# Performance work log

Hardware: AMD Instinct MI355X
Metric: run time of the kernel (lower is better)

The kernel has to match this reference:

```python
import jax, jax.numpy as jnp
import numpy as np

BN_EPS = 1e-5
RES_SCALE = 0.7


def setup_inputs() -> dict:
    key = jax.random.key(0)
    ks = jax.random.split(key, 10)
    N, IN_DIM, HID, E, L = 50000, 2000, 64, 1600000, 4
    features = jax.random.normal(ks[0], (N, IN_DIM), dtype=jnp.float32)
    edges = jax.random.randint(ks[1], (2, E), 0, N, dtype=jnp.int64)
    # GCNConv params: layer 0 is in_dim->hid, layers 1..3 are hid->hid
    W0 = jax.random.normal(ks[2], (IN_DIM, HID), dtype=jnp.float32) / np.sqrt(IN_DIM)
    b0 = jnp.zeros((HID,), dtype=jnp.float32)
    Wh = jax.random.normal(ks[3], (L - 1, HID, HID), dtype=jnp.float32) / np.sqrt(HID)
    bh = jnp.zeros((L - 1, HID), dtype=jnp.float32)
    # BatchNorm1d affine params per layer
    gamma = jnp.ones((L, HID), dtype=jnp.float32)
    beta = jnp.zeros((L, HID), dtype=jnp.float32)
    # learned layer-mixing weights (torch.randn init)
    lw = jax.random.normal(ks[4], (L,), dtype=jnp.float32)
    return {"features": features, "edges": edges, "W0": W0, "b0": b0,
            "Wh": Wh, "bh": bh, "gamma": gamma, "beta": beta, "lw": lw}


def reference(features, edges, W0, b0, Wh, bh, gamma, beta, lw):
    n = features.shape[0]
    src, dst = edges[0], edges[1]
    # GCN symmetric normalization with self-loops, edge_weight=1
    deg = jnp.zeros((n,), features.dtype).at[dst].add(1.0) + 1.0  # +1 self loop
    dinv = jax.lax.rsqrt(deg)
    enorm = dinv[src] * dinv[dst]       # [E]
    snorm = dinv * dinv                 # [N], self-loop norm

    def gcn_conv(x, W, b):
        xw = x @ W                                            # [N, H]
        agg = jnp.zeros_like(xw).at[dst].add(xw[src] * enorm[:, None])
        agg = agg + xw * snorm[:, None]
        return agg + b

    def batchnorm(x, g, bt):
        m = x.mean(axis=0)
        v = x.var(axis=0)  # biased variance, as in BN training normalization
        return (x - m) * jax.lax.rsqrt(v + BN_EPS) * g + bt

    L = gamma.shape[0]
    Ws = [W0] + [Wh[i] for i in range(L - 1)]
    bs = [b0] + [bh[i] for i in range(L - 1)]

    layer_out = []
    x = features
    for i in range(L):
        x = gcn_conv(x, Ws[i], bs[i])
        x = jax.nn.relu(batchnorm(x, gamma[i], beta[i]))
        if i > 0:
            x = x + RES_SCALE * layer_out[i - 1]
        layer_out.append(x)

    w = jax.nn.softmax(lw)
    emb = layer_out[0] * w[0]
    for i in range(1, L):
        emb = emb + layer_out[i] * w[i]
    return emb
```

## Files before the change

kernel.cpp:

```cpp
#include <hip/hip_runtime.h>
#include <hip/hip_bf16.h>
#include <math.h>

#define BN_EPS 1e-5f
#define RES_SCALE 0.7f

typedef float f4 __attribute__((ext_vector_type(4)));
typedef short s8 __attribute__((ext_vector_type(8)));

__device__ inline short f2bf(float f) {
    __hip_bfloat16 h = __float2bfloat16(f);
    return *reinterpret_cast<short*>(&h);
}

__device__ inline float bf2f(unsigned short u) {
    return __uint_as_float((unsigned)u << 16);
}

__global__ __launch_bounds__(256) void k_zero(int* counts, int* cursor, float* stats, int N, int S) {
    int i = blockIdx.x * 256 + threadIdx.x;
    if (i < N) { counts[i] = 0; cursor[i] = 0; }
    if (i < S) stats[i] = 0.0f;
}

__global__ __launch_bounds__(256) void k_count(const int* __restrict__ edges, int E, int* __restrict__ counts) {
    int e = blockIdx.x * 256 + threadIdx.x;
    if (e < E) atomicAdd(&counts[edges[E + e]], 1);
}

__global__ __launch_bounds__(256) void k_dinv(const int* __restrict__ counts, float* __restrict__ dinv, int N) {
    int i = blockIdx.x * 256 + threadIdx.x;
    if (i < N) dinv[i] = rsqrtf((float)counts[i] + 1.0f);
}

__global__ __launch_bounds__(256) void k_scan1(const int* __restrict__ counts, int* __restrict__ bsum, int N) {
    __shared__ int sd[256];
    int t = threadIdx.x;
    int base = blockIdx.x * 1024 + t * 4;
    int s = 0;
    if (base + 3 < N) { int4 v = *(const int4*)(counts + base); s = v.x + v.y + v.z + v.w; }
    else { for (int j = 0; j < 4; ++j) if (base + j < N) s += counts[base + j]; }
    sd[t] = s; __syncthreads();
    for (int off = 128; off > 0; off >>= 1) { if (t < off) sd[t] += sd[t + off]; __syncthreads(); }
    if (t == 0) bsum[blockIdx.x] = sd[0];
}

__global__ void k_scan2(int* bsum, int B, int* rowstart, int N) {
    if (threadIdx.x == 0 && blockIdx.x == 0) {
        int run = 0;
        for (int b = 0; b < B; ++b) { int v = bsum[b]; bsum[b] = run; run += v; }
        rowstart[N] = run;
    }
}

__global__ __launch_bounds__(256) void k_scan3(const int* __restrict__ counts, const int* __restrict__ bsum,
                                               int* __restrict__ rowstart, int N) {
    __shared__ int sd[256];
    int t = threadIdx.x;
    int base = blockIdx.x * 1024 + t * 4;
    int v0 = 0, v1 = 0, v2 = 0, v3 = 0;
    if (base + 3 < N) { int4 v = *(const int4*)(counts + base); v0 = v.x; v1 = v.y; v2 = v.z; v3 = v.w; }
    else {
        if (base < N) v0 = counts[base];
        if (base + 1 < N) v1 = counts[base + 1];
        if (base + 2 < N) v2 = counts[base + 2];
        if (base + 3 < N) v3 = counts[base + 3];
    }
    int s = v0 + v1 + v2 + v3;
    sd[t] = s; __syncthreads();
    for (int off = 1; off < 256; off <<= 1) {
        int add = (t >= off) ? sd[t - off] : 0;
        __syncthreads();
        sd[t] += add;
        __syncthreads();
    }
    int excl = sd[t] - s + bsum[blockIdx.x];
    if (base < N)     rowstart[base]     = excl;
    if (base + 1 < N) rowstart[base + 1] = excl + v0;
    if (base + 2 < N) rowstart[base + 2] = excl + v0 + v1;
    if (base + 3 < N) rowstart[base + 3] = excl + v0 + v1 + v2;
}

__global__ __launch_bounds__(256) void k_scatter(const int* __restrict__ edges, int E,
                                                 const int* __restrict__ rowstart, int* __restrict__ cursor,
                                                 int* __restrict__ colA) {
    int e = blockIdx.x * 256 + threadIdx.x;
    if (e >= E) return;
    int s = edges[e], d = edges[E + e];
    int pos = rowstart[d] + atomicAdd(&cursor[d], 1);
    colA[pos] = s;
}

__global__ __launch_bounds__(256) void k_wt(const float* __restrict__ W0, const float* __restrict__ Wh,
                                            short* __restrict__ WT0, short* __restrict__ WTh, int K0) {
    __shared__ short Ts[64][72];
    int b = blockIdx.x, t = threadIdx.x;
    int nk0 = (K0 + 63) >> 6;
    const float* W; short* dst; int K, kt;
    if (b < nk0) { W = W0; dst = WT0; K = K0; kt = b * 64; }
    else { int l = b - nk0; W = Wh + (size_t)l * 64 * 64; dst = WTh + (size_t)l * 64 * 64; K = 64; kt = 0; }
    #pragma unroll
    for (int i = 0; i < 16; ++i) {
        int idx = t + i * 256;
        int r = idx >> 6, c = idx & 63;
        int gk = kt + r;
        Ts[c][r] = (gk < K) ? f2bf(W[(size_t)gk * 64 + c]) : (short)0;
    }
    __syncthreads();
    #pragma unroll
    for (int i = 0; i < 16; ++i) {
        int idx = t + i * 256;
        int n = idx >> 6, r = idx & 63;
        int gk = kt + r;
        if (gk < K) dst[(size_t)n * K + gk] = Ts[n][r];
    }
}

__global__ __launch_bounds__(256) void k_mm(const float* __restrict__ X, const short* __restrict__ WT,
                                            const float* __restrict__ dinv,
                                            __hip_bfloat16* __restrict__ Cb, int N, int K) {
    __shared__ float Xs[64][36];
    __shared__ short Ws[64][40];
    int t = threadIdx.x;
    int w = t >> 6, lane = t & 63;
    int m = lane & 15, kq = lane >> 4;
    int row0 = blockIdx.x * 64;

    int xr = t >> 3, xc = t & 7;
    int wn = t >> 2, wc = t & 3;

    f4 acc[4] = {};
    f4 px0, px1; int4 pw;

    {
        int gr0 = row0 + xr, gr1 = row0 + xr + 32, gk = xc * 4;
        px0 = (gr0 < N && gk < K) ? *(const f4*)(X + (size_t)gr0 * K + gk) : (f4){};
        px1 = (gr1 < N && gk < K) ? *(const f4*)(X + (size_t)gr1 * K + gk) : (f4){};
        int gkw = wc * 8;
        pw = (gkw < K) ? *(const int4*)(WT + (size_t)wn * K + gkw) : make_int4(0, 0, 0, 0);
    }

    for (int kt = 0; kt < K; kt += 32) {
        *(f4*)&Xs[xr][xc * 4] = px0;
        *(f4*)&Xs[xr + 32][xc * 4] = px1;
        *(int4*)&Ws[wn][wc * 8] = pw;
        __syncthreads();

        int kn = kt + 32;
        if (kn < K) {
            int gr0 = row0 + xr, gr1 = row0 + xr + 32, gk = kn + xc * 4;
            px0 = (gr0 < N && gk < K) ? *(const f4*)(X + (size_t)gr0 * K + gk) : (f4){};
            px1 = (gr1 < N && gk < K) ? *(const f4*)(X + (size_t)gr1 * K + gk) : (f4){};
            int gkw = kn + wc * 8;
            pw = (gkw < K) ? *(const int4*)(WT + (size_t)wn * K + gkw) : make_int4(0, 0, 0, 0);
        }

        f4 a0 = *(const f4*)&Xs[w * 16 + m][kq * 8];
        f4 a1 = *(const f4*)&Xs[w * 16 + m][kq * 8 + 4];
        s8 av;
        #pragma unroll
        for (int j = 0; j < 4; ++j) { av[j] = f2bf(a0[j]); av[j + 4] = f2bf(a1[j]); }
        #pragma unroll
        for (int ct = 0; ct < 4; ++ct) {
            s8 bv = *(const s8*)&Ws[ct * 16 + m][kq * 8];
            acc[ct] = __builtin_amdgcn_mfma_f32_16x16x32_bf16(av, bv, acc[ct], 0, 0, 0);
        }
        __syncthreads();
    }

    #pragma unroll
    for (int reg = 0; reg < 4; ++reg) {
        int gr = row0 + w * 16 + kq * 4 + reg;
        if (gr < N) {
            float di = dinv[gr];
            #pragma unroll
            for (int ct = 0; ct < 4; ++ct)
                Cb[(size_t)gr * 64 + ct * 16 + m] = __float2bfloat16(acc[ct][reg] * di);
        }
    }
}

__global__ __launch_bounds__(256) void k_gather(const __hip_bfloat16* __restrict__ xw, const int* __restrict__ colA,
                                                const int* __restrict__ rowstart,
                                                const float* __restrict__ dinv, float* __restrict__ agg, int N) {
    int wave = (blockIdx.x * 256 + threadIdx.x) >> 6;
    int lane = threadIdx.x & 63;
    if (wave >= N) return;
    int r = wave;
    const unsigned short* xwu = (const unsigned short*)xw;
    float acc = bf2f(xwu[(size_t)r * 64 + lane]);
    int b = rowstart[r], e = rowstart[r + 1];
    for (int base = b; base < e; base += 64) {
        int idx = base + lane;
        int c = (idx < e) ? colA[idx] : 0;
        int cnt = min(64, e - base);
        int j = 0;
        for (; j + 7 < cnt; j += 8) {
            int s0 = __builtin_amdgcn_readlane(c, j);
            int s1 = __builtin_amdgcn_readlane(c, j + 1);
            int s2 = __builtin_amdgcn_readlane(c, j + 2);
            int s3 = __builtin_amdgcn_readlane(c, j + 3);
            int s4 = __builtin_amdgcn_readlane(c, j + 4);
            int s5 = __builtin_amdgcn_readlane(c, j + 5);
            int s6 = __builtin_amdgcn_readlane(c, j + 6);
            int s7 = __builtin_amdgcn_readlane(c, j + 7);
            float v0 = bf2f(xwu[(size_t)s0 * 64 + lane]);
            float v1 = bf2f(xwu[(size_t)s1 * 64 + lane]);
            float v2 = bf2f(xwu[(size_t)s2 * 64 + lane]);
            float v3 = bf2f(xwu[(size_t)s3 * 64 + lane]);
            float v4 = bf2f(xwu[(size_t)s4 * 64 + lane]);
            float v5 = bf2f(xwu[(size_t)s5 * 64 + lane]);
            float v6 = bf2f(xwu[(size_t)s6 * 64 + lane]);
            float v7 = bf2f(xwu[(size_t)s7 * 64 + lane]);
            acc += ((v0 + v1) + (v2 + v3)) + ((v4 + v5) + (v6 + v7));
        }
        for (; j < cnt; ++j) {
            int s = __builtin_amdgcn_readlane(c, j);
            acc += bf2f(xwu[(size_t)s * 64 + lane]);
        }
    }
    agg[(size_t)r * 64 + lane] = acc * dinv[r];
}

__global__ __launch_bounds__(256) void k_stats(const float* __restrict__ x, float* __restrict__ stats, int N) {
    int col = threadIdx.x & 63;
    int sub = threadIdx.x >> 6;
    float s = 0.f, s2 = 0.f;
    for (int r = blockIdx.x * 4 + sub; r < N; r += gridDim.x * 4) {
        float v = x[(size_t)r * 64 + col];
        s += v; s2 += v * v;
    }
    __shared__ float sd[2][4][64];
    sd[0][sub][col] = s; sd[1][sub][col] = s2;
    __syncthreads();
    if (sub == 0) {
        s  = sd[0][0][col] + sd[0][1][col] + sd[0][2][col] + sd[0][3][col];
        s2 = sd[1][0][col] + sd[1][1][col] + sd[1][2][col] + sd[1][3][col];
        atomicAdd(&stats[col], s);
        atomicAdd(&stats[64 + col], s2);
    }
}

__global__ __launch_bounds__(256) void k_elem(const float* __restrict__ agg, const float* __restrict__ stats,
                                              const float* __restrict__ gamma, const float* __restrict__ beta,
                                              const float* __restrict__ lw, const float* __restrict__ xprev,
                                              float* __restrict__ xcur, float* __restrict__ emb,
                                              int N, int layer, int L) {
    int i = blockIdx.x * 256 + threadIdx.x;
    if (i >= N * 64) return;
    int c = i & 63;
    float rN = 1.0f / (float)N;
    float mn = stats[c] * rN;
    float var = stats[64 + c] * rN - mn * mn;
    float inv = rsqrtf(var + BN_EPS);
    float v = (agg[i] - mn) * inv * gamma[c] + beta[c];
    v = fmaxf(v, 0.0f);
    if (layer > 0) v += RES_SCALE * xprev[i];
    xcur[i] = v;
    float mx = lw[0];
    for (int j = 1; j < L; ++j) mx = fmaxf(mx, lw[j]);
    float sum = 0.f, wl = 0.f;
    for (int j = 0; j < L; ++j) {
        float e = __expf(lw[j] - mx);
        sum += e;
        if (j == layer) wl = e;
    }
    wl /= sum;
    float prev = (layer == 0) ? 0.0f : emb[i];
    emb[i] = prev + wl * v;
}

extern "C" void kernel_launch(void* const* d_in, const int* in_sizes, int n_in,
                              void* d_out, int out_size, void* d_ws, size_t ws_size,
                              hipStream_t stream) {
    const float* features = (const float*)d_in[0];
    const int*   edges    = (const int*)d_in[1];
    const float* W0       = (const float*)d_in[2];
    const float* Wh       = (const float*)d_in[4];
    const float* gamma    = (const float*)d_in[6];
    const float* beta     = (const float*)d_in[7];
    const float* lw       = (const float*)d_in[8];

    const int HID    = in_sizes[3];
    const int IN_DIM = in_sizes[2] / HID;
    const int N      = in_sizes[0] / IN_DIM;
    const int E      = in_sizes[1] / 2;
    const int L      = in_sizes[8];
    float* out = (float*)d_out;

    char* ws = (char*)d_ws;
    auto alloc = [&](size_t bytes) { char* p = ws; ws += (bytes + 255) & ~(size_t)255; return p; };
    int*   counts   = (int*)alloc((size_t)N * 4);
    int*   cursor   = (int*)alloc((size_t)N * 4);
    int*   rowstart = (int*)alloc((size_t)(N + 1) * 4);
    int*   bsum     = (int*)alloc(256 * 4);
    float* dinv     = (float*)alloc((size_t)N * 4);
    float* stats    = (float*)alloc((size_t)L * 128 * 4);
    int*   colA     = (int*)alloc((size_t)E * 4);
    short* WT0      = (short*)alloc((size_t)HID * IN_DIM * 2);
    short* WTh      = (short*)alloc((size_t)(L - 1) * HID * HID * 2);
    __hip_bfloat16* xw = (__hip_bfloat16*)alloc((size_t)N * HID * 2);
    float* agg      = (float*)alloc((size_t)N * HID * 4);
    float* x0       = (float*)alloc((size_t)N * HID * 4);
    float* x1       = (float*)alloc((size_t)N * HID * 4);

    int S = L * 128;
    int zgrid = (max(N, S) + 255) / 256;
    k_zero<<<zgrid, 256, 0, stream>>>(counts, cursor, stats, N, S);

    int egrid = (E + 255) / 256;
    int ngrid = (N + 255) / 256;
    k_count<<<egrid, 256, 0, stream>>>(edges, E, counts);
    k_dinv<<<ngrid, 256, 0, stream>>>(counts, dinv, N);

    int B = (N + 1023) / 1024;
    k_scan1<<<B, 256, 0, stream>>>(counts, bsum, N);
    k_scan2<<<1, 64, 0, stream>>>(bsum, B, rowstart, N);
    k_scan3<<<B, 256, 0, stream>>>(counts, bsum, rowstart, N);
    k_scatter<<<egrid, 256, 0, stream>>>(edges, E, rowstart, cursor, colA);

    int nk0 = (IN_DIM + 63) / 64;
    k_wt<<<nk0 + (L - 1), 256, 0, stream>>>(W0, Wh, WT0, WTh, IN_DIM);

    int mmgrid = (N + 63) / 64;
    int ggrid  = (N + 3) / 4;
    int elgrid = ((size_t)N * HID + 255) / 256;

    const float* xc_prev = nullptr;
    for (int l = 0; l < L; ++l) {
        const float* Xin = (l == 0) ? features : xc_prev;
        int K = (l == 0) ? IN_DIM : HID;
        const short* WTl = (l == 0) ? WT0 : WTh + (size_t)(l - 1) * HID * HID;
        k_mm<<<mmgrid, 256, 0, stream>>>(Xin, WTl, dinv, xw, N, K);
        k_gather<<<ggrid, 256, 0, stream>>>(xw, colA, rowstart, dinv, agg, N);
        k_stats<<<256, 256, 0, stream>>>(agg, stats + l * 128, N);
        float* xcur = (l % 2 == 0) ? x0 : x1;
        const float* xprev = (l == 0) ? nullptr : ((l % 2 == 0) ? x1 : x0);
        k_elem<<<elgrid, 256, 0, stream>>>(agg, stats + l * 128, gamma + l * HID, beta + l * HID,
                                           lw, xprev, xcur, out, N, l, L);
        xc_prev = xcur;
    }
}
```

Baseline: 1.053 ms.

## Pack gather loads in pairs, widen GEMM K-tile, vectorize elementwise, fuse dinv

```diff
diff --git a/kernel.cpp b/kernel.cpp
--- a/kernel.cpp
+++ b/kernel.cpp
@@ -11,10 +11,6 @@
 __device__ inline short f2bf(float f) {
     __hip_bfloat16 h = __float2bfloat16(f);
     return *reinterpret_cast<short*>(&h);
-}
-
-__device__ inline float bf2f(unsigned short u) {
-    return __uint_as_float((unsigned)u << 16);
 }
 
 __global__ __launch_bounds__(256) void k_zero(int* counts, int* cursor, float* stats, int N, int S) {
@@ -28,18 +24,28 @@
     if (e < E) atomicAdd(&counts[edges[E + e]], 1);
 }
 
-__global__ __launch_bounds__(256) void k_dinv(const int* __restrict__ counts, float* __restrict__ dinv, int N) {
-    int i = blockIdx.x * 256 + threadIdx.x;
-    if (i < N) dinv[i] = rsqrtf((float)counts[i] + 1.0f);
-}
-
-__global__ __launch_bounds__(256) void k_scan1(const int* __restrict__ counts, int* __restrict__ bsum, int N) {
+__global__ __launch_bounds__(256) void k_scan1(const int* __restrict__ counts, int* __restrict__ bsum,
+                                               float* __restrict__ dinv, int N) {
     __shared__ int sd[256];
     int t = threadIdx.x;
     int base = blockIdx.x * 1024 + t * 4;
     int s = 0;
-    if (base + 3 < N) { int4 v = *(const int4*)(counts + base); s = v.x + v.y + v.z + v.w; }
-    else { for (int j = 0; j < 4; ++j) if (base + j < N) s += counts[base + j]; }
+    if (base + 3 < N) {
+        int4 v = *(const int4*)(counts + base);
+        s = v.x + v.y + v.z + v.w;
+        f4 d;
+        d.x = rsqrtf((float)v.x + 1.0f);
+        d.y = rsqrtf((float)v.y + 1.0f);
+        d.z = rsqrtf((float)v.z + 1.0f);
+        d.w = rsqrtf((float)v.w + 1.0f);
+        *(f4*)(dinv + base) = d;
+    } else {
+        for (int j = 0; j < 4; ++j) if (base + j < N) {
+            int cv = counts[base + j];
+            s += cv;
+            dinv[base + j] = rsqrtf((float)cv + 1.0f);
+        }
+    }
     sd[t] = s; __syncthreads();
     for (int off = 128; off > 0; off >>= 1) { if (t < off) sd[t] += sd[t + off]; __syncthreads(); }
     if (t == 0) bsum[blockIdx.x] = sd[0];
@@ -119,8 +125,8 @@
 __global__ __launch_bounds__(256) void k_mm(const float* __restrict__ X, const short* __restrict__ WT,
                                             const float* __restrict__ dinv,
                                             __hip_bfloat16* __restrict__ Cb, int N, int K) {
-    __shared__ float Xs[64][36];
-    __shared__ short Ws[64][40];
+    __shared__ float Xs[64][68];
+    __shared__ short Ws[64][72];
     int t = threadIdx.x;
     int w = t >> 6, lane = t & 63;
     int m = lane & 15, kq = lane >> 4;
@@ -130,40 +136,59 @@
     int wn = t >> 2, wc = t & 3;
 
     f4 acc[4] = {};
-    f4 px0, px1; int4 pw;
+    f4 px0, px1, px2, px3; int4 pw0, pw1;
 
     {
-        int gr0 = row0 + xr, gr1 = row0 + xr + 32, gk = xc * 4;
-        px0 = (gr0 < N && gk < K) ? *(const f4*)(X + (size_t)gr0 * K + gk) : (f4){};
-        px1 = (gr1 < N && gk < K) ? *(const f4*)(X + (size_t)gr1 * K + gk) : (f4){};
-        int gkw = wc * 8;
-        pw = (gkw < K) ? *(const int4*)(WT + (size_t)wn * K + gkw) : make_int4(0, 0, 0, 0);
-    }
-
-    for (int kt = 0; kt < K; kt += 32) {
-        *(f4*)&Xs[xr][xc * 4] = px0;
-        *(f4*)&Xs[xr + 32][xc * 4] = px1;
-        *(int4*)&Ws[wn][wc * 8] = pw;
+        int gr0 = row0 + xr, gr1 = row0 + xr + 32;
+        int gk0 = xc * 4, gk1 = 32 + xc * 4;
+        px0 = (gr0 < N && gk0 < K) ? *(const f4*)(X + (size_t)gr0 * K + gk0) : (f4){};
+        px1 = (gr0 < N && gk1 < K) ? *(const f4*)(X + (size_t)gr0 * K + gk1) : (f4){};
+        px2 = (gr1 < N && gk0 < K) ? *(const f4*)(X + (size_t)gr1 * K + gk0) : (f4){};
+        px3 = (gr1 < N && gk1 < K) ? *(const f4*)(X + (size_t)gr1 * K + gk1) : (f4){};
+        int gw0 = wc * 8, gw1 = 32 + wc * 8;
+        pw0 = (gw0 < K) ? *(const int4*)(WT + (size_t)wn * K + gw0) : make_int4(0, 0, 0, 0);
+        pw1 = (gw1 < K) ? *(const int4*)(WT + (size_t)wn * K + gw1) : make_int4(0, 0, 0, 0);
+    }
+
+    for (int kt = 0; kt < K; kt += 64) {
+        *(f4*)&Xs[xr][xc * 4]           = px0;
+        *(f4*)&Xs[xr][32 + xc * 4]      = px1;
+        *(f4*)&Xs[xr + 32][xc * 4]      = px2;
+        *(f4*)&Xs[xr + 32][32 + xc * 4] = px3;
+        *(int4*)&Ws[wn][wc * 8]         = pw0;
+        *(int4*)&Ws[wn][32 + wc * 8]    = pw1;
         __syncthreads();
 
-        int kn = kt + 32;
+        int kn = kt + 64;
         if (kn < K) {
-            int gr0 = row0 + xr, gr1 = row0 + xr + 32, gk = kn + xc * 4;
-            px0 = (gr0 < N && gk < K) ? *(const f4*)(X + (size_t)gr0 * K + gk) : (f4){};
-            px1 = (gr1 < N && gk < K) ? *(const f4*)(X + (size_t)gr1 * K + gk) : (f4){};
-            int gkw = kn + wc * 8;
-            pw = (gkw < K) ? *(const int4*)(WT + (size_t)wn * K + gkw) : make_int4(0, 0, 0, 0);
-        }
-
-        f4 a0 = *(const f4*)&Xs[w * 16 + m][kq * 8];
-        f4 a1 = *(const f4*)&Xs[w * 16 + m][kq * 8 + 4];
-        s8 av;
+            int gr0 = row0 + xr, gr1 = row0 + xr + 32;
+            int gk0 = kn + xc * 4, gk1 = kn + 32 + xc * 4;
+            px0 = (gr0 < N && gk0 < K) ? *(const f4*)(X + (size_t)gr0 * K + gk0) : (f4){};
+            px1 = (gr0 < N && gk1 < K) ? *(const f4*)(X + (size_t)gr0 * K + gk1) : (f4){};
+            px2 = (gr1 < N && gk0 < K) ? *(const f4*)(X + (size_t)gr1 * K + gk0) : (f4){};
+            px3 = (gr1 < N && gk1 < K) ? *(const f4*)(X + (size_t)gr1 * K + gk1) : (f4){};
+            int gw0 = kn + wc * 8, gw1 = kn + 32 + wc * 8;
+            pw0 = (gw0 < K) ? *(const int4*)(WT + (size_t)wn * K + gw0) : make_int4(0, 0, 0, 0);
+            pw1 = (gw1 < K) ? *(const int4*)(WT + (size_t)wn * K + gw1) : make_int4(0, 0, 0, 0);
+        }
+
+        int arow = w * 16 + m;
+        f4 a00 = *(const f4*)&Xs[arow][kq * 8];
+        f4 a01 = *(const f4*)&Xs[arow][kq * 8 + 4];
+        f4 a10 = *(const f4*)&Xs[arow][32 + kq * 8];
+        f4 a11 = *(const f4*)&Xs[arow][32 + kq * 8 + 4];
+        s8 av0, av1;
         #pragma unroll
-        for (int j = 0; j < 4; ++j) { av[j] = f2bf(a0[j]); av[j + 4] = f2bf(a1[j]); }
+        for (int j = 0; j < 4; ++j) {
+            av0[j] = f2bf(a00[j]); av0[j + 4] = f2bf(a01[j]);
+            av1[j] = f2bf(a10[j]); av1[j + 4] = f2bf(a11[j]);
+        }
         #pragma unroll
         for (int ct = 0; ct < 4; ++ct) {
-            s8 bv = *(const s8*)&Ws[ct * 16 + m][kq * 8];
-            acc[ct] = __builtin_amdgcn_mfma_f32_16x16x32_bf16(av, bv, acc[ct], 0, 0, 0);
+            s8 bv0 = *(const s8*)&Ws[ct * 16 + m][kq * 8];
+            s8 bv1 = *(const s8*)&Ws[ct * 16 + m][32 + kq * 8];
+            acc[ct] = __builtin_amdgcn_mfma_f32_16x16x32_bf16(av0, bv0, acc[ct], 0, 0, 0);
+            acc[ct] = __builtin_amdgcn_mfma_f32_16x16x32_bf16(av1, bv1, acc[ct], 0, 0, 0);
         }
         __syncthreads();
     }
@@ -180,6 +205,12 @@
     }
 }
 
+__device__ inline const unsigned* g_rowsel(const unsigned* xw32, int c, int p, bool lo32) {
+    unsigned o0 = (unsigned)__builtin_amdgcn_readlane(c, 2 * p) << 5;
+    unsigned o1 = (unsigned)__builtin_amdgcn_readlane(c, 2 * p + 1) << 5;
+    return xw32 + (lo32 ? o0 : o1);
+}
+
 __global__ __launch_bounds__(256) void k_gather(const __hip_bfloat16* __restrict__ xw, const int* __restrict__ colA,
                                                 const int* __restrict__ rowstart,
                                                 const float* __restrict__ dinv, float* __restrict__ agg, int N) {
@@ -187,39 +218,51 @@
     int lane = threadIdx.x & 63;
     if (wave >= N) return;
     int r = wave;
-    const unsigned short* xwu = (const unsigned short*)xw;
-    float acc = bf2f(xwu[(size_t)r * 64 + lane]);
+    const unsigned* xw32 = (const unsigned*)xw;
+    int l31 = lane & 31;
+    bool lo32 = lane < 32;
+
+    unsigned vs = xw32[((size_t)(unsigned)r << 5) | l31];
+    float acc0 = lo32 ? __uint_as_float(vs << 16) : 0.0f;
+    float acc1 = lo32 ? __uint_as_float(vs & 0xffff0000u) : 0.0f;
+
     int b = rowstart[r], e = rowstart[r + 1];
     for (int base = b; base < e; base += 64) {
         int idx = base + lane;
         int c = (idx < e) ? colA[idx] : 0;
         int cnt = min(64, e - base);
+        int npair = cnt >> 1;
         int j = 0;
-        for (; j + 7 < cnt; j += 8) {
-            int s0 = __builtin_amdgcn_readlane(c, j);
-            int s1 = __builtin_amdgcn_readlane(c, j + 1);
-            int s2 = __builtin_amdgcn_readlane(c, j + 2);
-            int s3 = __builtin_amdgcn_readlane(c, j + 3);
-            int s4 = __builtin_amdgcn_readlane(c, j + 4);
-            int s5 = __builtin_amdgcn_readlane(c, j + 5);
-            int s6 = __builtin_amdgcn_readlane(c, j + 6);
-            int s7 = __builtin_amdgcn_readlane(c, j + 7);
-            float v0 = bf2f(xwu[(size_t)s0 * 64 + lane]);
-            float v1 = bf2f(xwu[(size_t)s1 * 64 + lane]);
-            float v2 = bf2f(xwu[(size_t)s2 * 64 + lane]);
-            float v3 = bf2f(xwu[(size_t)s3 * 64 + lane]);
-            float v4 = bf2f(xwu[(size_t)s4 * 64 + lane]);
-            float v5 = bf2f(xwu[(size_t)s5 * 64 + lane]);
-            float v6 = bf2f(xwu[(size_t)s6 * 64 + lane]);
-            float v7 = bf2f(xwu[(size_t)s7 * 64 + lane]);
-            acc += ((v0 + v1) + (v2 + v3)) + ((v4 + v5) + (v6 + v7));
-        }
-        for (; j < cnt; ++j) {
-            int s = __builtin_amdgcn_readlane(c, j);
-            acc += bf2f(xwu[(size_t)s * 64 + lane]);
-        }
-    }
-    agg[(size_t)r * 64 + lane] = acc * dinv[r];
+        for (; j + 3 < npair; j += 4) {
+            unsigned v0 = g_rowsel(xw32, c, j,     lo32)[l31];
+            unsigned v1 = g_rowsel(xw32, c, j + 1, lo32)[l31];
+            unsigned v2 = g_rowsel(xw32, c, j + 2, lo32)[l31];
+            unsigned v3 = g_rowsel(xw32, c, j + 3, lo32)[l31];
+            acc0 += __uint_as_float(v0 << 16); acc1 += __uint_as_float(v0 & 0xffff0000u);
+            acc0 += __uint_as_float(v1 << 16); acc1 += __uint_as_float(v1 & 0xffff0000u);
+            acc0 += __uint_as_float(v2 << 16); acc1 += __uint_as_float(v2 & 0xffff0000u);
+            acc0 += __uint_as_float(v3 << 16); acc1 += __uint_as_float(v3 & 0xffff0000u);
+        }
+        for (; j < npair; ++j) {
+            unsigned v = g_rowsel(xw32, c, j, lo32)[l31];
+            acc0 += __uint_as_float(v << 16); acc1 += __uint_as_float(v & 0xffff0000u);
+        }
+        if (cnt & 1) {
+            int s = __builtin_amdgcn_readlane(c, cnt - 1);
+            unsigned v = xw32[((size_t)(unsigned)s << 5) | l31];
+            if (lo32) {
+                acc0 += __uint_as_float(v << 16);
+                acc1 += __uint_as_float(v & 0xffff0000u);
+            }
+        }
+    }
+    acc0 += __shfl_xor(acc0, 32);
+    acc1 += __shfl_xor(acc1, 32);
+    if (lo32) {
+        float di = dinv[r];
+        float2 o; o.x = acc0 * di; o.y = acc1 * di;
+        *(float2*)(agg + ((size_t)r << 6) + l31 * 2) = o;
+    }
 }
 
 __global__ __launch_bounds__(256) void k_stats(const float* __restrict__ x, float* __restrict__ stats, int N) {
@@ -246,28 +289,49 @@
                                               const float* __restrict__ lw, const float* __restrict__ xprev,
                                               float* __restrict__ xcur, float* __restrict__ emb,
                                               int N, int layer, int L) {
-    int i = blockIdx.x * 256 + threadIdx.x;
-    if (i >= N * 64) return;
-    int c = i & 63;
+    size_t i = ((size_t)blockIdx.x * 256 + threadIdx.x) * 4;
+    if (i >= (size_t)N * 64) return;
+    int c = (int)(i & 63);
     float rN = 1.0f / (float)N;
-    float mn = stats[c] * rN;
-    float var = stats[64 + c] * rN - mn * mn;
-    float inv = rsqrtf(var + BN_EPS);
-    float v = (agg[i] - mn) * inv * gamma[c] + beta[c];
-    v = fmaxf(v, 0.0f);
-    if (layer > 0) v += RES_SCALE * xprev[i];
-    xcur[i] = v;
+    f4 av = *(const f4*)(agg + i);
+    f4 gv = *(const f4*)(gamma + c);
+    f4 bv = *(const f4*)(beta + c);
+    f4 sv = *(const f4*)(stats + c);
+    f4 qv = *(const f4*)(stats + 64 + c);
+    f4 v;
+    #pragma unroll
+    for (int j = 0; j < 4; ++j) {
+        float mn = sv[j] * rN;
+        float var = qv[j] * rN - mn * mn;
+        float inv = rsqrtf(var + BN_EPS);
+        v[j] = fmaxf((av[j] - mn) * inv * gv[j] + bv[j], 0.0f);
+    }
+    f4 xp = {};
+    if (layer > 0) {
+        xp = *(const f4*)(xprev + i);
+        #pragma unroll
+        for (int j = 0; j < 4; ++j) v[j] += RES_SCALE * xp[j];
+    }
+    if (layer < L - 1) *(f4*)(xcur + i) = v;
+    if (layer == 0) return;
+
     float mx = lw[0];
     for (int j = 1; j < L; ++j) mx = fmaxf(mx, lw[j]);
-    float sum = 0.f, wl = 0.f;
-    for (int j = 0; j < L; ++j) {
-        float e = __expf(lw[j] - mx);
-        sum += e;
-        if (j == layer) wl = e;
-    }
-    wl /= sum;
-    float prev = (layer == 0) ? 0.0f : emb[i];
-    emb[i] = prev + wl * v;
+    float sum = 0.f, wbuf[8];
+    for (int j = 0; j < L; ++j) { float ee = __expf(lw[j] - mx); wbuf[j] = ee; sum += ee; }
+    float rs = 1.0f / sum;
+    float wl = wbuf[layer] * rs;
+    f4 o;
+    if (layer == 1) {
+        float w0 = wbuf[0] * rs;
+        #pragma unroll
+        for (int j = 0; j < 4; ++j) o[j] = w0 * xp[j] + wl * v[j];
+    } else {
+        f4 ep = *(const f4*)(emb + i);
+        #pragma unroll
+        for (int j = 0; j < 4; ++j) o[j] = ep[j] + wl * v[j];
+    }
+    *(f4*)(emb + i) = o;
 }
 
 extern "C" void kernel_launch(void* const* d_in, const int* in_sizes, int n_in,
@@ -309,12 +373,10 @@
     k_zero<<<zgrid, 256, 0, stream>>>(counts, cursor, stats, N, S);
 
     int egrid = (E + 255) / 256;
-    int ngrid = (N + 255) / 256;
     k_count<<<egrid, 256, 0, stream>>>(edges, E, counts);
-    k_dinv<<<ngrid, 256, 0, stream>>>(counts, dinv, N);
 
     int B = (N + 1023) / 1024;
-    k_scan1<<<B, 256, 0, stream>>>(counts, bsum, N);
+    k_scan1<<<B, 256, 0, stream>>>(counts, bsum, dinv, N);
     k_scan2<<<1, 64, 0, stream>>>(bsum, B, rowstart, N);
     k_scan3<<<B, 256, 0, stream>>>(counts, bsum, rowstart, N);
     k_scatter<<<egrid, 256, 0, stream>>>(edges, E, rowstart, cursor, colA);
@@ -324,8 +386,9 @@
 
     int mmgrid = (N + 63) / 64;
     int ggrid  = (N + 3) / 4;
-    int elgrid = ((size_t)N * HID + 255) / 256;
-
+    int elgrid = (int)(((size_t)N * HID / 4 + 255) / 256);
+
+    float* xb[2] = { x0, x1 };
     const float* xc_prev = nullptr;
     for (int l = 0; l < L; ++l) {
         const float* Xin = (l == 0) ? features : xc_prev;
@@ -334,10 +397,10 @@
         k_mm<<<mmgrid, 256, 0, stream>>>(Xin, WTl, dinv, xw, N, K);
         k_gather<<<ggrid, 256, 0, stream>>>(xw, colA, rowstart, dinv, agg, N);
         k_stats<<<256, 256, 0, stream>>>(agg, stats + l * 128, N);
-        float* xcur = (l % 2 == 0) ? x0 : x1;
-        const float* xprev = (l == 0) ? nullptr : ((l % 2 == 0) ? x1 : x0);
+        float* xcur = (l < L - 1) ? xb[l & 1] : nullptr;
+        const float* xprev = (l == 0) ? nullptr : xb[(l - 1) & 1];
         k_elem<<<elgrid, 256, 0, stream>>>(agg, stats + l * 128, gamma + l * HID, beta + l * HID,
                                            lw, xprev, xcur, out, N, l, L);
-        xc_prev = xcur;
-    }
-}
+        if (l < L - 1) xc_prev = xcur;
+    }
+}
```

Measured after the change: 1.006 ms. 1.05x faster.
